# Kernel tuning notes

Hardware: AMD Instinct MI355X
Metric: run time of the kernel (lower is better)

## Reference

```python
import jax, jax.numpy as jnp
import numpy as np

N_NODES = 200000
N_EDGES = 6400000
IN_FEAT = 128
HIDDEN = 16


def gcn_conv(x, W, b, row, col, n):
    # PyG GCNConv: h = X W ; out_i = sum_{(j->i)} d_j^{-1/2} d_i^{-1/2} h_j + b
    # (row = source j, col = target i; self-loops already included in row/col)
    deg = jax.ops.segment_sum(jnp.ones_like(col, dtype=x.dtype), col, num_segments=n)
    dinv = jnp.where(deg > 0, jax.lax.rsqrt(deg), jnp.zeros_like(deg))
    norm = dinv[row] * dinv[col]            # [E+N]
    h = x @ W                               # [N, out] small GEMM
    msg = norm[:, None] * h[row]            # gather over edges
    out = jax.ops.segment_sum(msg, col, num_segments=n)  # scatter-add to targets
    return out + b


def setup_inputs() -> dict:
    key = jax.random.key(0)
    k1, k2, k3, k4 = jax.random.split(key, 4)
    x = jax.random.normal(k1, (N_NODES, IN_FEAT), dtype=jnp.float32)
    edge_index = jax.random.randint(k2, (2, N_EDGES), 0, N_NODES, dtype=jnp.int32)
    # Glorot-ish init for the two linear layers
    W1 = jax.random.normal(k3, (IN_FEAT, HIDDEN), dtype=jnp.float32) / np.sqrt(IN_FEAT)
    W2 = jax.random.normal(k4, (HIDDEN, 1), dtype=jnp.float32) / np.sqrt(HIDDEN)
    b1 = jnp.zeros((HIDDEN,), dtype=jnp.float32)
    b2 = jnp.zeros((1,), dtype=jnp.float32)
    return {"x": x, "edge_index": edge_index, "W1": W1, "b1": b1, "W2": W2, "b2": b2}


def reference(x, edge_index, W1, b1, W2, b2):
    n = x.shape[0]
    # add self-loops (as PyG GCNConv does by default)
    loop = jnp.arange(n, dtype=edge_index.dtype)
    row = jnp.concatenate([edge_index[0], loop])
    col = jnp.concatenate([edge_index[1], loop])
    h = gcn_conv(x, W1, b1, row, col, n)    # [N, 16]
    h = jax.nn.relu(h)
    out = gcn_conv(h, W2, b2, row, col, n)  # [N, 1]
    return out.squeeze(-1)                  # [N]
```

## Files before the change

kernel.cpp:

```cpp
#include <hip/hip_runtime.h>
#include <hip/hip_fp16.h>

#define N_NODES 200000
#define N_EDGES 6400000
#define IN_FEAT 128
#define HIDDEN  16

#define RN 512
#define CSHIFT 9
#define NC 391
#define CAPB 18432
#define SRC_MASK 0x3FFFFu
#define SB1 8192
#define NBLK 782
#define NSLOT (NC * (RN + 1))

typedef float v4f __attribute__((ext_vector_type(4)));
typedef _Float16 f16x8 __attribute__((ext_vector_type(8)));
typedef float f32x4 __attribute__((ext_vector_type(4)));


__global__ void k_init(unsigned* __restrict__ ccur) {
    int b = blockIdx.x * 256 + threadIdx.x;
    if (b < NC) ccur[b] = (unsigned)b * CAPB;
}


__global__ __launch_bounds__(512) void k_cscat(const int* __restrict__ row,
                                               const int* __restrict__ col,
                                               unsigned* __restrict__ ccur,
                                               unsigned* __restrict__ tmp1) {
    __shared__ unsigned cnt[512], s[512], cur[512], gdst[512];
    __shared__ unsigned buf[SB1];
    __shared__ unsigned short bkt[SB1];
    const long long e0 = (long long)blockIdx.x * SB1;
    long long rem = (long long)N_EDGES - e0;
    const int n = rem > SB1 ? SB1 : (int)rem;
    const int t = threadIdx.x;
    cnt[t] = 0u;
    __syncthreads();

    const int4* c4 = (const int4*)(col + e0);
    for (int i = t; i < n / 4; i += 512) {
        int4 v = c4[i];
        atomicAdd(&cnt[(unsigned)v.x >> CSHIFT], 1u);
        atomicAdd(&cnt[(unsigned)v.y >> CSHIFT], 1u);
        atomicAdd(&cnt[(unsigned)v.z >> CSHIFT], 1u);
        atomicAdd(&cnt[(unsigned)v.w >> CSHIFT], 1u);
    }
    __syncthreads();

    unsigned cv = cnt[t];
    s[t] = cv;
    __syncthreads();
    #pragma unroll
    for (int d = 1; d < 512; d <<= 1) {
        unsigned add = (t >= d) ? s[t - d] : 0u;
        __syncthreads();
        s[t] += add;
        __syncthreads();
    }
    cur[t] = s[t] - cv;
    __syncthreads();

    for (int i = t; i < n; i += 512) {
        unsigned c = (unsigned)col[e0 + i];
        unsigned sr = (unsigned)row[e0 + i];
        unsigned b = c >> CSHIFT;
        unsigned pos = atomicAdd(&cur[b], 1u);
        buf[pos] = ((c & (RN - 1u)) << 18) | sr;
        bkt[pos] = (unsigned short)b;
    }
    if (t < NC) gdst[t] = cnt[t] ? atomicAdd(&ccur[t], cnt[t]) : 0u;
    __syncthreads();

    for (int i = t; i < n; i += 512) {
        unsigned b = bkt[i];
        unsigned base = s[b] - cnt[b];
        unsigned dest = gdst[b] + ((unsigned)i - base);
        if (dest < (b + 1u) * CAPB) tmp1[dest] = buf[i];
    }
}


__global__ __launch_bounds__(1024) void k_bsort(const unsigned* __restrict__ tmp1,
                                                const unsigned* __restrict__ ccur,
                                                unsigned* __restrict__ boffs,
                                                float* __restrict__ dinv,
                                                unsigned* __restrict__ sorted) {
    __shared__ unsigned dcnt[RN], dcur[RN], sscan[RN];
    const int r = blockIdx.x;
    const unsigned lo = (unsigned)r * CAPB;
    unsigned fill = ccur[r] - lo;
    if (fill > CAPB) fill = CAPB;
    const unsigned hi = lo + fill;
    const unsigned node0 = (unsigned)r * RN;
    const unsigned slot0 = (unsigned)r * (RN + 1);
    if (threadIdx.x < RN) dcnt[threadIdx.x] = 0u;
    __syncthreads();

    for (unsigned i = lo + threadIdx.x; i < hi; i += 1024)
        atomicAdd(&dcnt[tmp1[i] >> 18], 1u);
    __syncthreads();

    unsigned c = 0;
    if (threadIdx.x < RN) { c = dcnt[threadIdx.x]; sscan[threadIdx.x] = c; }
    __syncthreads();
    #pragma unroll
    for (int d = 1; d < RN; d <<= 1) {
        unsigned add = 0;
        if (threadIdx.x < RN && threadIdx.x >= d) add = sscan[threadIdx.x - d];
        __syncthreads();
        if (threadIdx.x < RN) sscan[threadIdx.x] += add;
        __syncthreads();
    }
    if (threadIdx.x < RN) {
        unsigned excl = sscan[threadIdx.x] - c;
        dcur[threadIdx.x] = excl;
        boffs[slot0 + threadIdx.x] = lo + excl;
        unsigned node = node0 + threadIdx.x;
        if (node < N_NODES) dinv[node] = rsqrtf((float)c + 1.0f);
    }
    if (threadIdx.x == 0) boffs[slot0 + RN] = hi;
    __syncthreads();

    unsigned i = lo + threadIdx.x;
    for (; i + 7168 < hi; i += 8192) {
        unsigned p0 = tmp1[i];
        unsigned p1 = tmp1[i + 1024];
        unsigned p2 = tmp1[i + 2048];
        unsigned p3 = tmp1[i + 3072];
        unsigned p4 = tmp1[i + 4096];
        unsigned p5 = tmp1[i + 5120];
        unsigned p6 = tmp1[i + 6144];
        unsigned p7 = tmp1[i + 7168];
        unsigned q0 = atomicAdd(&dcur[p0 >> 18], 1u);
        unsigned q1 = atomicAdd(&dcur[p1 >> 18], 1u);
        unsigned q2 = atomicAdd(&dcur[p2 >> 18], 1u);
        unsigned q3 = atomicAdd(&dcur[p3 >> 18], 1u);
        unsigned q4 = atomicAdd(&dcur[p4 >> 18], 1u);
        unsigned q5 = atomicAdd(&dcur[p5 >> 18], 1u);
        unsigned q6 = atomicAdd(&dcur[p6 >> 18], 1u);
        unsigned q7 = atomicAdd(&dcur[p7 >> 18], 1u);
        sorted[lo + q0] = p0 & SRC_MASK;
        sorted[lo + q1] = p1 & SRC_MASK;
        sorted[lo + q2] = p2 & SRC_MASK;
        sorted[lo + q3] = p3 & SRC_MASK;
        sorted[lo + q4] = p4 & SRC_MASK;
        sorted[lo + q5] = p5 & SRC_MASK;
        sorted[lo + q6] = p6 & SRC_MASK;
        sorted[lo + q7] = p7 & SRC_MASK;
    }
    for (; i < hi; i += 1024) {
        unsigned p = tmp1[i];
        unsigned pos = atomicAdd(&dcur[p >> 18], 1u);
        sorted[lo + pos] = p & SRC_MASK;
    }
}


__global__ __launch_bounds__(256) void k_gemm1(const float* __restrict__ x,
                                               const float* __restrict__ W1,
                                               const float* __restrict__ dinv,
                                               __half* __restrict__ h16) {
    const int wave = (blockIdx.x * 256 + threadIdx.x) >> 6;
    const int lane = threadIdx.x & 63;
    const int m16 = lane & 15;
    const int quad = lane >> 4;
    if (wave * 16 >= N_NODES) return;

    f16x8 bf[4];
    #pragma unroll
    for (int kb = 0; kb < 4; ++kb)
        #pragma unroll
        for (int j = 0; j < 8; ++j)
            bf[kb][j] = (_Float16)W1[(kb * 32 + quad * 8 + j) * HIDDEN + m16];

    const int node0 = wave * 16;
    const float* xrow = x + (size_t)(node0 + m16) * IN_FEAT + quad * 8;
    f32x4 acc = {0.f, 0.f, 0.f, 0.f};
    #pragma unroll
    for (int kb = 0; kb < 4; ++kb) {
        const v4f* p = (const v4f*)(xrow + kb * 32);
        v4f u0 = p[0], u1 = p[1];
        f16x8 af;
        af[0] = (_Float16)u0.x; af[1] = (_Float16)u0.y;
        af[2] = (_Float16)u0.z; af[3] = (_Float16)u0.w;
        af[4] = (_Float16)u1.x; af[5] = (_Float16)u1.y;
        af[6] = (_Float16)u1.z; af[7] = (_Float16)u1.w;
        acc = __builtin_amdgcn_mfma_f32_16x16x32_f16(af, bf[kb], acc, 0, 0, 0);
    }
    #pragma unroll
    for (int r = 0; r < 4; ++r) {
        int node = node0 + quad * 4 + r;
        h16[(size_t)node * HIDDEN + m16] = __float2half(dinv[node] * acc[r]);
    }
}


__global__ __launch_bounds__(256) void k_agg1(const unsigned* __restrict__ sorted,
                                              const unsigned* __restrict__ boffs,
                                              const uint2* __restrict__ h16v,
                                              const float* __restrict__ dinv,
                                              const float* __restrict__ b1,
                                              const float* __restrict__ W2,
                                              float* __restrict__ tp) {
    const unsigned tid = blockIdx.x * 256 + threadIdx.x;
    const unsigned node = tid >> 3;
    const int l = tid & 7;
    const int q = l & 3;
    const int eh = l >> 2;
    if (node >= N_NODES) return;

    const unsigned slot = node + (node >> CSHIFT);
    unsigned e = boffs[slot];
    const unsigned o1 = boffs[slot + 1];
    float a0 = 0.f, a1 = 0.f, a2 = 0.f, a3 = 0.f;

    unsigned nb0, nb1, nb2, nb3, nb4, nb5, nb6, nb7;
    bool have = (e + 16 <= o1);
    if (have) {
        nb0 = sorted[e +  0 + eh]; nb1 = sorted[e +  2 + eh];
        nb2 = sorted[e +  4 + eh]; nb3 = sorted[e +  6 + eh];
        nb4 = sorted[e +  8 + eh]; nb5 = sorted[e + 10 + eh];
        nb6 = sorted[e + 12 + eh]; nb7 = sorted[e + 14 + eh];
    }
    while (have) {
        unsigned cb0 = nb0, cb1 = nb1, cb2 = nb2, cb3 = nb3;
        unsigned cb4 = nb4, cb5 = nb5, cb6 = nb6, cb7 = nb7;
        e += 16;
        have = (e + 16 <= o1);
        if (have) {
            nb0 = sorted[e +  0 + eh]; nb1 = sorted[e +  2 + eh];
            nb2 = sorted[e +  4 + eh]; nb3 = sorted[e +  6 + eh];
            nb4 = sorted[e +  8 + eh]; nb5 = sorted[e + 10 + eh];
            nb6 = sorted[e + 12 + eh]; nb7 = sorted[e + 14 + eh];
        }
        uint2 v0 = h16v[(size_t)cb0 * 4 + q];
        uint2 v1 = h16v[(size_t)cb1 * 4 + q];
        uint2 v2 = h16v[(size_t)cb2 * 4 + q];
        uint2 v3 = h16v[(size_t)cb3 * 4 + q];
        uint2 v4 = h16v[(size_t)cb4 * 4 + q];
        uint2 v5 = h16v[(size_t)cb5 * 4 + q];
        uint2 v6 = h16v[(size_t)cb6 * 4 + q];
        uint2 v7 = h16v[(size_t)cb7 * 4 + q];
        float2 f, g;
        f = __half22float2(*(const __half2*)&v0.x); g = __half22float2(*(const __half2*)&v0.y);
        a0 += f.x; a1 += f.y; a2 += g.x; a3 += g.y;
        f = __half22float2(*(const __half2*)&v1.x); g = __half22float2(*(const __half2*)&v1.y);
        a0 += f.x; a1 += f.y; a2 += g.x; a3 += g.y;
        f = __half22float2(*(const __half2*)&v2.x); g = __half22float2(*(const __half2*)&v2.y);
        a0 += f.x; a1 += f.y; a2 += g.x; a3 += g.y;
        f = __half22float2(*(const __half2*)&v3.x); g = __half22float2(*(const __half2*)&v3.y);
        a0 += f.x; a1 += f.y; a2 += g.x; a3 += g.y;
        f = __half22float2(*(const __half2*)&v4.x); g = __half22float2(*(const __half2*)&v4.y);
        a0 += f.x; a1 += f.y; a2 += g.x; a3 += g.y;
        f = __half22float2(*(const __half2*)&v5.x); g = __half22float2(*(const __half2*)&v5.y);
        a0 += f.x; a1 += f.y; a2 += g.x; a3 += g.y;
        f = __half22float2(*(const __half2*)&v6.x); g = __half22float2(*(const __half2*)&v6.y);
        a0 += f.x; a1 += f.y; a2 += g.x; a3 += g.y;
        f = __half22float2(*(const __half2*)&v7.x); g = __half22float2(*(const __half2*)&v7.y);
        a0 += f.x; a1 += f.y; a2 += g.x; a3 += g.y;
    }
    if (e + 8 <= o1) {
        unsigned cb0 = sorted[e + 0 + eh], cb1 = sorted[e + 2 + eh];
        unsigned cb2 = sorted[e + 4 + eh], cb3 = sorted[e + 6 + eh];
        uint2 v0 = h16v[(size_t)cb0 * 4 + q];
        uint2 v1 = h16v[(size_t)cb1 * 4 + q];
        uint2 v2 = h16v[(size_t)cb2 * 4 + q];
        uint2 v3 = h16v[(size_t)cb3 * 4 + q];
        float2 f, g;
        f = __half22float2(*(const __half2*)&v0.x); g = __half22float2(*(const __half2*)&v0.y);
        a0 += f.x; a1 += f.y; a2 += g.x; a3 += g.y;
        f = __half22float2(*(const __half2*)&v1.x); g = __half22float2(*(const __half2*)&v1.y);
        a0 += f.x; a1 += f.y; a2 += g.x; a3 += g.y;
        f = __half22float2(*(const __half2*)&v2.x); g = __half22float2(*(const __half2*)&v2.y);
        a0 += f.x; a1 += f.y; a2 += g.x; a3 += g.y;
        f = __half22float2(*(const __half2*)&v3.x); g = __half22float2(*(const __half2*)&v3.y);
        a0 += f.x; a1 += f.y; a2 += g.x; a3 += g.y;
        e += 8;
    }
    for (; e < o1; ++e) {
        if (eh == 0) {
            unsigned s = sorted[e];
            uint2 v = h16v[(size_t)s * 4 + q];
            float2 f = __half22float2(*(const __half2*)&v.x);
            float2 g = __half22float2(*(const __half2*)&v.y);
            a0 += f.x; a1 += f.y; a2 += g.x; a3 += g.y;
        }
    }

    a0 += __shfl_xor(a0, 4, 8);
    a1 += __shfl_xor(a1, 4, 8);
    a2 += __shfl_xor(a2, 4, 8);
    a3 += __shfl_xor(a3, 4, 8);

    uint2 vs = h16v[(size_t)node * 4 + q];
    float2 s01 = __half22float2(*(const __half2*)&vs.x);
    float2 s23 = __half22float2(*(const __half2*)&vs.y);
    float di = dinv[node];
    float p0 = fmaf(di, a0 + s01.x, b1[4 * q + 0]);
    float p1 = fmaf(di, a1 + s01.y, b1[4 * q + 1]);
    float p2 = fmaf(di, a2 + s23.x, b1[4 * q + 2]);
    float p3 = fmaf(di, a3 + s23.y, b1[4 * q + 3]);
    float r = fmaxf(p0, 0.f) * W2[4 * q + 0] + fmaxf(p1, 0.f) * W2[4 * q + 1]
            + fmaxf(p2, 0.f) * W2[4 * q + 2] + fmaxf(p3, 0.f) * W2[4 * q + 3];
    r += __shfl_xor(r, 2, 8);
    r += __shfl_xor(r, 1, 8);
    if (l == 0) tp[node] = di * r;
}


__global__ __launch_bounds__(256) void k_agg2(const unsigned* __restrict__ sorted,
                                              const unsigned* __restrict__ boffs,
                                              const float* __restrict__ tp,
                                              const float* __restrict__ dinv,
                                              const float* __restrict__ b2,
                                              float* __restrict__ out) {
    const unsigned node = blockIdx.x * 256 + threadIdx.x;
    if (node >= N_NODES) return;

    const unsigned slot = node + (node >> CSHIFT);
    unsigned e = boffs[slot];
    const unsigned o1 = boffs[slot + 1];
    float acc = 0.f;

    unsigned n0, n1, n2, n3, n4, n5, n6, n7;
    bool have = (e + 8 <= o1);
    if (have) {
        n0 = sorted[e];     n1 = sorted[e + 1]; n2 = sorted[e + 2]; n3 = sorted[e + 3];
        n4 = sorted[e + 4]; n5 = sorted[e + 5]; n6 = sorted[e + 6]; n7 = sorted[e + 7];
    }
    while (have) {
        unsigned c0 = n0, c1 = n1, c2 = n2, c3 = n3, c4 = n4, c5 = n5, c6 = n6, c7 = n7;
        e += 8;
        have = (e + 8 <= o1);
        if (have) {
            n0 = sorted[e];     n1 = sorted[e + 1]; n2 = sorted[e + 2]; n3 = sorted[e + 3];
            n4 = sorted[e + 4]; n5 = sorted[e + 5]; n6 = sorted[e + 6]; n7 = sorted[e + 7];
        }
        float t0 = tp[c0], t1 = tp[c1], t2 = tp[c2], t3 = tp[c3];
        float t4 = tp[c4], t5 = tp[c5], t6 = tp[c6], t7 = tp[c7];
        acc += t0 + t1 + t2 + t3;
        acc += t4 + t5 + t6 + t7;
    }
    for (; e < o1; ++e) acc += tp[sorted[e]];

    out[node] = fmaf(dinv[node], tp[node] + acc, b2[0]);
}


extern "C" void kernel_launch(void* const* d_in, const int* in_sizes, int n_in,
                              void* d_out, int out_size, void* d_ws, size_t ws_size,
                              hipStream_t stream) {
    const float* x   = (const float*)d_in[0];
    const int*   ei  = (const int*)d_in[1];
    const float* W1  = (const float*)d_in[2];
    const float* b1  = (const float*)d_in[3];
    const float* W2  = (const float*)d_in[4];
    const float* b2  = (const float*)d_in[5];
    float* out = (float*)d_out;

    const int* row = ei;
    const int* col = ei + N_EDGES;

    unsigned* ccur   = (unsigned*)d_ws;
    unsigned* boffs  = ccur + 512;
    float*    dinv   = (float*)(boffs + NSLOT + 73);
    float*    tp     = dinv + N_NODES;
    __half*   h16    = (__half*)(tp + N_NODES);
    unsigned* tmp1   = (unsigned*)(h16 + (size_t)N_NODES * HIDDEN);
    unsigned* sorted = tmp1 + (size_t)NC * CAPB;

    k_init<<<2, 256, 0, stream>>>(ccur);
    k_cscat<<<NBLK, 512, 0, stream>>>(row, col, ccur, tmp1);
    k_bsort<<<NC, 1024, 0, stream>>>(tmp1, ccur, boffs, dinv, sorted);
    k_gemm1<<<(N_NODES / 16 + 3) / 4, 256, 0, stream>>>(x, W1, dinv, h16);
    k_agg1<<<(N_NODES * 8 + 255) / 256, 256, 0, stream>>>(sorted, boffs, (const uint2*)h16,
                                                          dinv, b1, W2, tp);
    k_agg2<<<(N_NODES + 255) / 256, 256, 0, stream>>>(sorted, boffs, tp, dinv, b2, out);
}
```

Baseline: 373.6 us.

## Split layer-1 feature table into two halves aggregated in separate passes

The fp16 hidden table is split into two 8-feature halves (16 bytes per node each), and layer-1 aggregation runs as two passes, each gathering one half. This shrinks the per-pass gather working set (3.2 MB instead of 6.4 MB) so it fits better in cache. The cost is reading the CSR edge list twice. Index loads are also switched to nontemporal, and the bucket-cursor init kernel is replaced by a memset with relative offsets.

```diff
diff --git a/kernel.cpp b/kernel.cpp
--- a/kernel.cpp
+++ b/kernel.cpp
@@ -19,11 +19,7 @@
 typedef _Float16 f16x8 __attribute__((ext_vector_type(8)));
 typedef float f32x4 __attribute__((ext_vector_type(4)));
 
-
-__global__ void k_init(unsigned* __restrict__ ccur) {
-    int b = blockIdx.x * 256 + threadIdx.x;
-    if (b < NC) ccur[b] = (unsigned)b * CAPB;
-}
+#define NTL(p) __builtin_nontemporal_load(p)
 
 
 __global__ __launch_bounds__(512) void k_cscat(const int* __restrict__ row,
@@ -71,7 +67,7 @@
         buf[pos] = ((c & (RN - 1u)) << 18) | sr;
         bkt[pos] = (unsigned short)b;
     }
-    if (t < NC) gdst[t] = cnt[t] ? atomicAdd(&ccur[t], cnt[t]) : 0u;
+    if (t < NC) gdst[t] = cnt[t] ? (unsigned)t * CAPB + atomicAdd(&ccur[t], cnt[t]) : 0u;
     __syncthreads();
 
     for (int i = t; i < n; i += 512) {
@@ -91,7 +87,7 @@
     __shared__ unsigned dcnt[RN], dcur[RN], sscan[RN];
     const int r = blockIdx.x;
     const unsigned lo = (unsigned)r * CAPB;
-    unsigned fill = ccur[r] - lo;
+    unsigned fill = ccur[r];
     if (fill > CAPB) fill = CAPB;
     const unsigned hi = lo + fill;
     const unsigned node0 = (unsigned)r * RN;
@@ -162,7 +158,8 @@
 __global__ __launch_bounds__(256) void k_gemm1(const float* __restrict__ x,
                                                const float* __restrict__ W1,
                                                const float* __restrict__ dinv,
-                                               __half* __restrict__ h16) {
+                                               __half* __restrict__ hlo,
+                                               __half* __restrict__ hhi) {
     const int wave = (blockIdx.x * 256 + threadIdx.x) >> 6;
     const int lane = threadIdx.x & 63;
     const int m16 = lane & 15;
@@ -190,26 +187,30 @@
         af[6] = (_Float16)u1.z; af[7] = (_Float16)u1.w;
         acc = __builtin_amdgcn_mfma_f32_16x16x32_f16(af, bf[kb], acc, 0, 0, 0);
     }
+    __half* htab = (m16 < 8) ? hlo : hhi;
+    const int f = m16 & 7;
     #pragma unroll
     for (int r = 0; r < 4; ++r) {
         int node = node0 + quad * 4 + r;
-        h16[(size_t)node * HIDDEN + m16] = __float2half(dinv[node] * acc[r]);
-    }
-}
-
-
-__global__ __launch_bounds__(256) void k_agg1(const unsigned* __restrict__ sorted,
+        htab[(size_t)node * 8 + f] = __float2half(dinv[node] * acc[r]);
+    }
+}
+
+
+__global__ __launch_bounds__(256) void k_aggh(const unsigned* __restrict__ sorted,
                                               const unsigned* __restrict__ boffs,
-                                              const uint2* __restrict__ h16v,
+                                              const uint2* __restrict__ htab,
                                               const float* __restrict__ dinv,
-                                              const float* __restrict__ b1,
-                                              const float* __restrict__ W2,
-                                              float* __restrict__ tp) {
+                                              const float* __restrict__ b1h,
+                                              const float* __restrict__ W2h,
+                                              const float* __restrict__ tprev,
+                                              float* __restrict__ tout,
+                                              int final_pass) {
     const unsigned tid = blockIdx.x * 256 + threadIdx.x;
     const unsigned node = tid >> 3;
     const int l = tid & 7;
-    const int q = l & 3;
-    const int eh = l >> 2;
+    const int q = l & 1;
+    const int eh = l >> 1;
     if (node >= N_NODES) return;
 
     const unsigned slot = node + (node >> CSHIFT);
@@ -218,32 +219,32 @@
     float a0 = 0.f, a1 = 0.f, a2 = 0.f, a3 = 0.f;
 
     unsigned nb0, nb1, nb2, nb3, nb4, nb5, nb6, nb7;
-    bool have = (e + 16 <= o1);
+    bool have = (e + 32 <= o1);
     if (have) {
-        nb0 = sorted[e +  0 + eh]; nb1 = sorted[e +  2 + eh];
-        nb2 = sorted[e +  4 + eh]; nb3 = sorted[e +  6 + eh];
-        nb4 = sorted[e +  8 + eh]; nb5 = sorted[e + 10 + eh];
-        nb6 = sorted[e + 12 + eh]; nb7 = sorted[e + 14 + eh];
+        nb0 = NTL(&sorted[e +  0 + eh]); nb1 = NTL(&sorted[e +  4 + eh]);
+        nb2 = NTL(&sorted[e +  8 + eh]); nb3 = NTL(&sorted[e + 12 + eh]);
+        nb4 = NTL(&sorted[e + 16 + eh]); nb5 = NTL(&sorted[e + 20 + eh]);
+        nb6 = NTL(&sorted[e + 24 + eh]); nb7 = NTL(&sorted[e + 28 + eh]);
     }
     while (have) {
         unsigned cb0 = nb0, cb1 = nb1, cb2 = nb2, cb3 = nb3;
         unsigned cb4 = nb4, cb5 = nb5, cb6 = nb6, cb7 = nb7;
-        e += 16;
-        have = (e + 16 <= o1);
+        e += 32;
+        have = (e + 32 <= o1);
         if (have) {
-            nb0 = sorted[e +  0 + eh]; nb1 = sorted[e +  2 + eh];
-            nb2 = sorted[e +  4 + eh]; nb3 = sorted[e +  6 + eh];
-            nb4 = sorted[e +  8 + eh]; nb5 = sorted[e + 10 + eh];
-            nb6 = sorted[e + 12 + eh]; nb7 = sorted[e + 14 + eh];
+            nb0 = NTL(&sorted[e +  0 + eh]); nb1 = NTL(&sorted[e +  4 + eh]);
+            nb2 = NTL(&sorted[e +  8 + eh]); nb3 = NTL(&sorted[e + 12 + eh]);
+            nb4 = NTL(&sorted[e + 16 + eh]); nb5 = NTL(&sorted[e + 20 + eh]);
+            nb6 = NTL(&sorted[e + 24 + eh]); nb7 = NTL(&sorted[e + 28 + eh]);
         }
-        uint2 v0 = h16v[(size_t)cb0 * 4 + q];
-        uint2 v1 = h16v[(size_t)cb1 * 4 + q];
-        uint2 v2 = h16v[(size_t)cb2 * 4 + q];
-        uint2 v3 = h16v[(size_t)cb3 * 4 + q];
-        uint2 v4 = h16v[(size_t)cb4 * 4 + q];
-        uint2 v5 = h16v[(size_t)cb5 * 4 + q];
-        uint2 v6 = h16v[(size_t)cb6 * 4 + q];
-        uint2 v7 = h16v[(size_t)cb7 * 4 + q];
+        uint2 v0 = htab[(size_t)cb0 * 2 + q];
+        uint2 v1 = htab[(size_t)cb1 * 2 + q];
+        uint2 v2 = htab[(size_t)cb2 * 2 + q];
+        uint2 v3 = htab[(size_t)cb3 * 2 + q];
+        uint2 v4 = htab[(size_t)cb4 * 2 + q];
+        uint2 v5 = htab[(size_t)cb5 * 2 + q];
+        uint2 v6 = htab[(size_t)cb6 * 2 + q];
+        uint2 v7 = htab[(size_t)cb7 * 2 + q];
         float2 f, g;
         f = __half22float2(*(const __half2*)&v0.x); g = __half22float2(*(const __half2*)&v0.y);
         a0 += f.x; a1 += f.y; a2 += g.x; a3 += g.y;
@@ -262,52 +263,43 @@
         f = __half22float2(*(const __half2*)&v7.x); g = __half22float2(*(const __half2*)&v7.y);
         a0 += f.x; a1 += f.y; a2 += g.x; a3 += g.y;
     }
-    if (e + 8 <= o1) {
-        unsigned cb0 = sorted[e + 0 + eh], cb1 = sorted[e + 2 + eh];
-        unsigned cb2 = sorted[e + 4 + eh], cb3 = sorted[e + 6 + eh];
-        uint2 v0 = h16v[(size_t)cb0 * 4 + q];
-        uint2 v1 = h16v[(size_t)cb1 * 4 + q];
-        uint2 v2 = h16v[(size_t)cb2 * 4 + q];
-        uint2 v3 = h16v[(size_t)cb3 * 4 + q];
-        float2 f, g;
-        f = __half22float2(*(const __half2*)&v0.x); g = __half22float2(*(const __half2*)&v0.y);
-        a0 += f.x; a1 += f.y; a2 += g.x; a3 += g.y;
-        f = __half22float2(*(const __half2*)&v1.x); g = __half22float2(*(const __half2*)&v1.y);
-        a0 += f.x; a1 += f.y; a2 += g.x; a3 += g.y;
-        f = __half22float2(*(const __half2*)&v2.x); g = __half22float2(*(const __half2*)&v2.y);
-        a0 += f.x; a1 += f.y; a2 += g.x; a3 += g.y;
-        f = __half22float2(*(const __half2*)&v3.x); g = __half22float2(*(const __half2*)&v3.y);
-        a0 += f.x; a1 += f.y; a2 += g.x; a3 += g.y;
-        e += 8;
+    for (; e + 4 <= o1; e += 4) {
+        unsigned s = NTL(&sorted[e + eh]);
+        uint2 v = htab[(size_t)s * 2 + q];
+        float2 f = __half22float2(*(const __half2*)&v.x);
+        float2 g = __half22float2(*(const __half2*)&v.y);
+        a0 += f.x; a1 += f.y; a2 += g.x; a3 += g.y;
     }
     for (; e < o1; ++e) {
         if (eh == 0) {
             unsigned s = sorted[e];
-            uint2 v = h16v[(size_t)s * 4 + q];
+            uint2 v = htab[(size_t)s * 2 + q];
             float2 f = __half22float2(*(const __half2*)&v.x);
             float2 g = __half22float2(*(const __half2*)&v.y);
             a0 += f.x; a1 += f.y; a2 += g.x; a3 += g.y;
         }
     }
 
-    a0 += __shfl_xor(a0, 4, 8);
-    a1 += __shfl_xor(a1, 4, 8);
-    a2 += __shfl_xor(a2, 4, 8);
-    a3 += __shfl_xor(a3, 4, 8);
-
-    uint2 vs = h16v[(size_t)node * 4 + q];
+    a0 += __shfl_xor(a0, 2, 8); a1 += __shfl_xor(a1, 2, 8);
+    a2 += __shfl_xor(a2, 2, 8); a3 += __shfl_xor(a3, 2, 8);
+    a0 += __shfl_xor(a0, 4, 8); a1 += __shfl_xor(a1, 4, 8);
+    a2 += __shfl_xor(a2, 4, 8); a3 += __shfl_xor(a3, 4, 8);
+
+    uint2 vs = htab[(size_t)node * 2 + q];
     float2 s01 = __half22float2(*(const __half2*)&vs.x);
     float2 s23 = __half22float2(*(const __half2*)&vs.y);
     float di = dinv[node];
-    float p0 = fmaf(di, a0 + s01.x, b1[4 * q + 0]);
-    float p1 = fmaf(di, a1 + s01.y, b1[4 * q + 1]);
-    float p2 = fmaf(di, a2 + s23.x, b1[4 * q + 2]);
-    float p3 = fmaf(di, a3 + s23.y, b1[4 * q + 3]);
-    float r = fmaxf(p0, 0.f) * W2[4 * q + 0] + fmaxf(p1, 0.f) * W2[4 * q + 1]
-            + fmaxf(p2, 0.f) * W2[4 * q + 2] + fmaxf(p3, 0.f) * W2[4 * q + 3];
-    r += __shfl_xor(r, 2, 8);
+    float p0 = fmaf(di, a0 + s01.x, b1h[4 * q + 0]);
+    float p1 = fmaf(di, a1 + s01.y, b1h[4 * q + 1]);
+    float p2 = fmaf(di, a2 + s23.x, b1h[4 * q + 2]);
+    float p3 = fmaf(di, a3 + s23.y, b1h[4 * q + 3]);
+    float r = fmaxf(p0, 0.f) * W2h[4 * q + 0] + fmaxf(p1, 0.f) * W2h[4 * q + 1]
+            + fmaxf(p2, 0.f) * W2h[4 * q + 2] + fmaxf(p3, 0.f) * W2h[4 * q + 3];
     r += __shfl_xor(r, 1, 8);
-    if (l == 0) tp[node] = di * r;
+    if (l == 0) {
+        if (final_pass) tout[node] = di * (r + tprev[node]);
+        else            tout[node] = r;
+    }
 }
 
 
@@ -328,23 +320,27 @@
     unsigned n0, n1, n2, n3, n4, n5, n6, n7;
     bool have = (e + 8 <= o1);
     if (have) {
-        n0 = sorted[e];     n1 = sorted[e + 1]; n2 = sorted[e + 2]; n3 = sorted[e + 3];
-        n4 = sorted[e + 4]; n5 = sorted[e + 5]; n6 = sorted[e + 6]; n7 = sorted[e + 7];
+        n0 = NTL(&sorted[e]);     n1 = NTL(&sorted[e + 1]);
+        n2 = NTL(&sorted[e + 2]); n3 = NTL(&sorted[e + 3]);
+        n4 = NTL(&sorted[e + 4]); n5 = NTL(&sorted[e + 5]);
+        n6 = NTL(&sorted[e + 6]); n7 = NTL(&sorted[e + 7]);
     }
     while (have) {
         unsigned c0 = n0, c1 = n1, c2 = n2, c3 = n3, c4 = n4, c5 = n5, c6 = n6, c7 = n7;
         e += 8;
         have = (e + 8 <= o1);
         if (have) {
-            n0 = sorted[e];     n1 = sorted[e + 1]; n2 = sorted[e + 2]; n3 = sorted[e + 3];
-            n4 = sorted[e + 4]; n5 = sorted[e + 5]; n6 = sorted[e + 6]; n7 = sorted[e + 7];
+            n0 = NTL(&sorted[e]);     n1 = NTL(&sorted[e + 1]);
+            n2 = NTL(&sorted[e + 2]); n3 = NTL(&sorted[e + 3]);
+            n4 = NTL(&sorted[e + 4]); n5 = NTL(&sorted[e + 5]);
+            n6 = NTL(&sorted[e + 6]); n7 = NTL(&sorted[e + 7]);
         }
         float t0 = tp[c0], t1 = tp[c1], t2 = tp[c2], t3 = tp[c3];
         float t4 = tp[c4], t5 = tp[c5], t6 = tp[c6], t7 = tp[c7];
         acc += t0 + t1 + t2 + t3;
         acc += t4 + t5 + t6 + t7;
     }
-    for (; e < o1; ++e) acc += tp[sorted[e]];
+    for (; e < o1; ++e) acc += tp[NTL(&sorted[e])];
 
     out[node] = fmaf(dinv[node], tp[node] + acc, b2[0]);
 }
@@ -367,16 +363,20 @@
     unsigned* ccur   = (unsigned*)d_ws;
     unsigned* boffs  = ccur + 512;
     float*    dinv   = (float*)(boffs + NSLOT + 73);
-    float*    tp     = dinv + N_NODES;
-    __half*   h16    = (__half*)(tp + N_NODES);
-    unsigned* tmp1   = (unsigned*)(h16 + (size_t)N_NODES * HIDDEN);
+    float*    tpA    = dinv + N_NODES;
+    float*    tp     = tpA + N_NODES;
+    __half*   hlo    = (__half*)(tp + N_NODES);
+    __half*   hhi    = hlo + (size_t)N_NODES * 8;
+    unsigned* tmp1   = (unsigned*)(hhi + (size_t)N_NODES * 8);
     unsigned* sorted = tmp1 + (size_t)NC * CAPB;
 
-    k_init<<<2, 256, 0, stream>>>(ccur);
+    (void)hipMemsetAsync(ccur, 0, 512 * sizeof(unsigned), stream);
     k_cscat<<<NBLK, 512, 0, stream>>>(row, col, ccur, tmp1);
     k_bsort<<<NC, 1024, 0, stream>>>(tmp1, ccur, boffs, dinv, sorted);
-    k_gemm1<<<(N_NODES / 16 + 3) / 4, 256, 0, stream>>>(x, W1, dinv, h16);
-    k_agg1<<<(N_NODES * 8 + 255) / 256, 256, 0, stream>>>(sorted, boffs, (const uint2*)h16,
-                                                          dinv, b1, W2, tp);
+    k_gemm1<<<(N_NODES / 16 + 3) / 4, 256, 0, stream>>>(x, W1, dinv, hlo, hhi);
+    k_aggh<<<(N_NODES * 8 + 255) / 256, 256, 0, stream>>>(sorted, boffs, (const uint2*)hlo,
+                                                          dinv, b1, W2, nullptr, tpA, 0);
+    k_aggh<<<(N_NODES * 8 + 255) / 256, 256, 0, stream>>>(sorted, boffs, (const uint2*)hhi,
+                                                          dinv, b1 + 8, W2 + 8, tpA, tp, 1);
     k_agg2<<<(N_NODES + 255) / 256, 256, 0, stream>>>(sorted, boffs, tp, dinv, b2, out);
 }
```

Result: slower. 483.6 us (+29.4%).
